# Kernel optimization log

Hardware: AMD Instinct MI355X
Metric: run time of the kernel (lower is better)

## Reference

```python
import jax, jax.numpy as jnp
import numpy as np

EPS = 0.5      # sinkhorn eps used by assign_batch_sinkhorn
NITERS = 15    # sinkhorn iterations used by assign_batch_sinkhorn


def pairwise_dists(features, centroids):
    # ||f - c|| via the expansion ||f||^2 + ||c||^2 - 2 f.c (avoids the
    # [B, nc, D] intermediate the naive broadcast would materialize).
    f2 = jnp.sum(features * features, axis=-1)          # [B]
    c2 = jnp.sum(centroids * centroids, axis=-1)        # [K]
    d2 = f2[:, None] + c2[None, :] - 2.0 * features @ centroids.T  # [B, K]
    return jnp.sqrt(jnp.maximum(d2, 0.0))


def sinkhorn(scores, eps=EPS, niters=NITERS):
    # Faithful to the torch sinkhorn(): Q = exp(scores/eps).T, normalize
    # columns (sum over K), then alternate row/column scalings.
    Q = jnp.exp(scores / eps).T                          # [K, B]
    Q = Q / jnp.sum(Q, axis=0, keepdims=True)
    K, B = Q.shape
    r = jnp.ones((K,), Q.dtype) / K
    c = jnp.ones((B,), Q.dtype) / B

    def body(_, Q):
        Q = Q * (r / jnp.sum(Q, axis=1))[:, None]
        Q = Q * (c / jnp.sum(Q, axis=0))[None, :]
        return Q

    Q = jax.lax.fori_loop(0, niters, body, Q)
    return (Q / jnp.sum(Q, axis=0, keepdims=True)).T     # [B, K]


def setup_inputs() -> dict:
    key = jax.random.key(0)
    kf, kc = jax.random.split(key)
    B, K, D = 16384, 2048, 1000
    # 0.1 scale keeps dists ~O(5) so exp(-dists/eps) stays in fp32 range
    # (unit-randn 1000-dim features give dists ~45 -> exp underflow).
    features = 0.1 * jax.random.normal(kf, (B, D), dtype=jnp.float32)
    centroids = 0.1 * jax.random.normal(kc, (K, D), dtype=jnp.float32)
    return {"features": features, "centroids": centroids}


def reference(features, centroids):
    B, K = features.shape[0], centroids.shape[0]
    dists = pairwise_dists(features, centroids)          # [B, K]

    # assign_batch_sinkhorn (soft assignments computed under no_grad)
    soft = jax.lax.stop_gradient(sinkhorn(-dists))       # [B, K]
    batch_assignments = jnp.argmin(soft, axis=1)         # [B] (as in source)
    soft_counts = jnp.sum(soft, axis=0)                  # [K]
    cluster_loss = jnp.mean(
        jnp.take_along_axis(dists, batch_assignments[:, None], axis=1))

    # the per-element python count loops, as fused scatter-adds
    cluster_counts = jnp.zeros((K,), jnp.int32).at[batch_assignments].add(1)
    raw_assign = jnp.argmin(dists, axis=1)
    raw_counts = jnp.zeros((K,), jnp.int32).at[raw_assign].add(1)

    return cluster_loss, batch_assignments, soft_counts, cluster_counts, raw_counts
```

## Files before the change

### kernel.cpp

```cpp
#include <hip/hip_runtime.h>

typedef __attribute__((ext_vector_type(8))) short bf16x8;
typedef __attribute__((ext_vector_type(8))) unsigned short ushort8_t;
typedef __attribute__((ext_vector_type(4))) float f32x4;

#define NB 16384
#define NK 2048
#define ND 1000
#define KP 1024
#define NCHK 1024

__device__ ushort g_E[(size_t)NB * NK];
__device__ ushort g_R[(size_t)NB * NK];
__device__ ushort g_Fh[(size_t)NB * KP], g_Fl[(size_t)NB * KP];
__device__ ushort g_Ch[(size_t)NK * KP], g_Cl[(size_t)NK * KP];
__device__ float  g_u[NK], g_c2[NK];
__device__ float  g_f2[NB], g_bd[NB];
__device__ float  g_part[(size_t)NCHK * NK];
__device__ int    g_cc[NK], g_rc[NK];

typedef const __attribute__((address_space(1))) void gvoid_t;
typedef __attribute__((address_space(3))) void lvoid_t;

union h16 { ushort u; _Float16 h; };

__device__ __forceinline__ ushort bf16_rne(float x){
    uint u = __float_as_uint(x);
    uint lsb = (u >> 16) & 1u;
    u += 0x7fffu + lsb;
    return (ushort)(u >> 16);
}
__device__ __forceinline__ float bf16_to_f(ushort h){
    return __uint_as_float(((uint)h) << 16);
}

__global__ __launch_bounds__(256) void cn_prep(const float* __restrict__ F,
                                               const float* __restrict__ Cn){
    const int isC = (blockIdx.x >= NB);
    const int row = isC ? (blockIdx.x - NB) : blockIdx.x;
    const float* __restrict__ X = isC ? Cn : F;
    ushort* __restrict__ H = isC ? g_Ch : g_Fh;
    ushort* __restrict__ L = isC ? g_Cl : g_Fl;
    float*  __restrict__ sq = isC ? g_c2 : g_f2;
    const int t = threadIdx.x;
    const int lane = t & 63, wid = t >> 6;
    if (isC && t == 0){ g_cc[row] = 0; g_rc[row] = 0; }
    float4 x = make_float4(0.f,0.f,0.f,0.f);
    if (t < 250) x = *(const float4*)(X + (size_t)row * ND + 4 * t);
    double s = (double)x.x*x.x + (double)x.y*x.y + (double)x.z*x.z + (double)x.w*x.w;
    ushort4 h4, l4;
#pragma unroll
    for (int c = 0; c < 4; ++c){
        float xc = (&x.x)[c];
        ushort h = bf16_rne(xc);
        (&h4.x)[c] = h;
        (&l4.x)[c] = bf16_rne(xc - bf16_to_f(h));
    }
    const int base = (t >> 3) << 5;
    const int grp  = (t >> 1) & 3;
    const int pos  = base + ((grp ^ ((row >> 1) & 3)) << 3) + ((4 * t) & 7);
    *(ushort4*)&H[(size_t)row * KP + pos] = h4;
    *(ushort4*)&L[(size_t)row * KP + pos] = l4;

    __shared__ double pr[4];
    for (int off = 32; off; off >>= 1) s += __shfl_xor(s, off);
    if (lane == 0) pr[wid] = s;
    __syncthreads();
    if (t == 0) sq[row] = (float)(pr[0] + pr[1] + pr[2] + pr[3]);
}

__global__ __launch_bounds__(256) void cn_gemm_dist(){
    __shared__ __attribute__((aligned(16))) ushort Ah[128 * 32];
    __shared__ __attribute__((aligned(16))) ushort Al[128 * 32];
    __shared__ __attribute__((aligned(16))) ushort Bh[128 * 32];
    __shared__ __attribute__((aligned(16))) ushort Bl[128 * 32];

    const int tid = threadIdx.x;
    const int lane = tid & 63, wid = tid >> 6;
    const int wr = wid >> 1, wc = wid & 1;
    const int brow0 = blockIdx.y * 128, bcol0 = blockIdx.x * 128;

    f32x4 acc[4][4];
#pragma unroll
    for (int m = 0; m < 4; ++m)
#pragma unroll
        for (int n = 0; n < 4; ++n) acc[m][n] = (f32x4){0.f,0.f,0.f,0.f};

    const int lrow = lane >> 2;
    const int lcol = (lane & 3) * 8;

    for (int step = 0; step < 32; ++step){
        const int k0 = step * 32;
#pragma unroll
        for (int i = 0; i < 2; ++i){
            const int ch = wid * 2 + i;
            const int ldso = ch * 512;
            const size_t ga = ((size_t)(brow0 + ch * 16 + lrow)) * KP + k0 + lcol;
            const size_t gb = ((size_t)(bcol0 + ch * 16 + lrow)) * KP + k0 + lcol;
            __builtin_amdgcn_global_load_lds((gvoid_t*)(g_Fh + ga), (lvoid_t*)(Ah + ldso), 16, 0, 0);
            __builtin_amdgcn_global_load_lds((gvoid_t*)(g_Fl + ga), (lvoid_t*)(Al + ldso), 16, 0, 0);
            __builtin_amdgcn_global_load_lds((gvoid_t*)(g_Ch + gb), (lvoid_t*)(Bh + ldso), 16, 0, 0);
            __builtin_amdgcn_global_load_lds((gvoid_t*)(g_Cl + gb), (lvoid_t*)(Bl + ldso), 16, 0, 0);
        }
        __syncthreads();

        const int arow = wr * 64 + (lane & 15);
        const int brow = wc * 64 + (lane & 15);
        const int kof  = (((lane >> 4) ^ ((lane >> 1) & 3)) * 8);
        bf16x8 afh[4], afl[4], bfh[4], bfl[4];
#pragma unroll
        for (int m = 0; m < 4; ++m){
            afh[m] = *(const bf16x8*)&Ah[(arow + m * 16) * 32 + kof];
            afl[m] = *(const bf16x8*)&Al[(arow + m * 16) * 32 + kof];
        }
#pragma unroll
        for (int n = 0; n < 4; ++n){
            bfh[n] = *(const bf16x8*)&Bh[(brow + n * 16) * 32 + kof];
            bfl[n] = *(const bf16x8*)&Bl[(brow + n * 16) * 32 + kof];
        }
#pragma unroll
        for (int m = 0; m < 4; ++m)
#pragma unroll
            for (int n = 0; n < 4; ++n){
                acc[m][n] = __builtin_amdgcn_mfma_f32_16x16x32_bf16(afh[m], bfh[n], acc[m][n], 0, 0, 0);
                acc[m][n] = __builtin_amdgcn_mfma_f32_16x16x32_bf16(afh[m], bfl[n], acc[m][n], 0, 0, 0);
                acc[m][n] = __builtin_amdgcn_mfma_f32_16x16x32_bf16(afl[m], bfh[n], acc[m][n], 0, 0, 0);
            }
        __syncthreads();
    }

#pragma unroll
    for (int m = 0; m < 4; ++m){
        int rowb = brow0 + wr * 64 + m * 16 + (lane >> 4) * 4;
#pragma unroll
        for (int n = 0; n < 4; ++n){
            int col = bcol0 + wc * 64 + n * 16 + (lane & 15);
            float c2v = g_c2[col];
#pragma unroll
            for (int j = 0; j < 4; ++j){
                float d2 = g_f2[rowb + j] + c2v - 2.0f * acc[m][n][j];
                float d  = sqrtf(fmaxf(d2, 0.0f));
                float e32 = __expf(-2.0f * d) * 8192.0f;
                size_t idx = (size_t)(rowb + j) * NK + col;
                h16 hv; hv.h = (_Float16)e32;
                float hf = (float)hv.h;
                h16 rv; rv.h = (_Float16)(e32 - hf);
                g_E[idx] = hv.u;
                g_R[idx] = rv.u;
            }
        }
    }
}

template<int MODE>
__global__ __launch_bounds__(256) void cn_sweep(float* __restrict__ outba){
    __shared__ float4 sred[3][8][64];
    const int lane = threadIdx.x & 63, wid = threadIdx.x >> 6;
    const int row0 = (blockIdx.x * 4 + wid) * 4;
    const float cst = (MODE == 0) ? 1.0f : (1.0f / (float)NB);

    float4 uu[8];
    if (MODE >= 1){
#pragma unroll
        for (int j = 0; j < 4; ++j)
#pragma unroll
            for (int h = 0; h < 2; ++h)
                uu[2 * j + h] = *(const float4*)&g_u[512 * j + 8 * lane + 4 * h];
    }

    float4 S[8];
#pragma unroll
    for (int j = 0; j < 8; ++j) S[j] = make_float4(0.f,0.f,0.f,0.f);

    for (int r = 0; r < 4; ++r){
        const int b = row0 + r;
        float tsum = 0.f;
        if (MODE <= 1){
            ushort8_t q8[4];
            const ushort* er = g_E + (size_t)b * NK + 8 * lane;
#pragma unroll
            for (int j = 0; j < 4; ++j){
                q8[j] = *(const ushort8_t*)(er + 512 * j);
#pragma unroll
                for (int c = 0; c < 8; ++c){
                    h16 cv; cv.u = q8[j][c];
                    float e = (float)cv.h;
                    tsum += (MODE == 1) ? e * (&uu[2 * j + (c >> 2)].x)[c & 3] : e;
                }
            }
#pragma unroll
            for (int off = 32; off; off >>= 1) tsum += __shfl_xor(tsum, off);
            const float v = cst / tsum;
#pragma unroll
            for (int j = 0; j < 4; ++j)
#pragma unroll
                for (int c = 0; c < 8; ++c){
                    h16 cv; cv.u = q8[j][c];
                    (&S[2 * j + (c >> 2)].x)[c & 3] += (float)cv.h * v;
                }
        } else {
            float ev[4][8];
            const ushort* er = g_E + (size_t)b * NK + 8 * lane;
            const ushort* rr = g_R + (size_t)b * NK + 8 * lane;
#pragma unroll
            for (int j = 0; j < 4; ++j){
                ushort8_t qe = *(const ushort8_t*)(er + 512 * j);
                ushort8_t qr = *(const ushort8_t*)(rr + 512 * j);
#pragma unroll
                for (int c = 0; c < 8; ++c){
                    h16 cv; cv.u = qe[c];
                    h16 rv; rv.u = qr[c];
                    float e = (float)cv.h + (float)rv.h;
                    ev[j][c] = e;
                    tsum += e * (&uu[2 * j + (c >> 2)].x)[c & 3];
                }
            }
#pragma unroll
            for (int off = 32; off; off >>= 1) tsum += __shfl_xor(tsum, off);
            const float v = cst / tsum;
#pragma unroll
            for (int j = 0; j < 4; ++j)
#pragma unroll
                for (int c = 0; c < 8; ++c)
                    (&S[2 * j + (c >> 2)].x)[c & 3] += ev[j][c] * v;

            if (MODE == 3){
                double bestW = 1.0e300; int bi = 0; float be = 1.f;
                float rbe = -1.f;      int ri = 0;
#pragma unroll
                for (int j = 0; j < 4; ++j){
#pragma unroll
                    for (int c = 0; c < 8; ++c){
                        int k = 512 * j + 8 * lane + c;
                        float e = ev[j][c];
                        double w = (double)e * (double)(&uu[2 * j + (c >> 2)].x)[c & 3];
                        if (w < bestW){ bestW = w; bi = k; be = e; }
                        if (e > rbe){ rbe = e; ri = k; }
                    }
                }
                for (int off = 32; off; off >>= 1){
                    double oW = __shfl_xor(bestW, off);
                    int    oi = __shfl_xor(bi, off);
                    float  oe = __shfl_xor(be, off);
                    if (oW < bestW || (oW == bestW && oi < bi)){ bestW = oW; bi = oi; be = oe; }
                    float ore = __shfl_xor(rbe, off);
                    int   ori = __shfl_xor(ri, off);
                    if (ore > rbe || (ore == rbe && ori < ri)){ rbe = ore; ri = ori; }
                }
                if (lane == 0){
                    outba[b] = (float)bi;
                    g_bd[b] = (float)(-0.5 * (log((double)be) - 9.010913347279288));
                    atomicAdd(&g_cc[bi], 1);
                    atomicAdd(&g_rc[ri], 1);
                }
            }
        }
    }

    if (wid > 0){
#pragma unroll
        for (int j = 0; j < 8; ++j) sred[wid - 1][j][lane] = S[j];
    }
    __syncthreads();
    if (wid == 0){
#pragma unroll
        for (int w = 0; w < 3; ++w)
#pragma unroll
            for (int j = 0; j < 8; ++j){
                float4 o = sred[w][j][lane];
                S[j].x += o.x; S[j].y += o.y; S[j].z += o.z; S[j].w += o.w;
            }
#pragma unroll
        for (int j = 0; j < 4; ++j)
#pragma unroll
            for (int h = 0; h < 2; ++h)
                *(float4*)&g_part[(size_t)blockIdx.x * NK + 512 * j + 8 * lane + 4 * h] = S[2 * j + h];
    }
}

__global__ __launch_bounds__(256) void cn_red0(){
    __shared__ double red[4][8];
    const int kk  = threadIdx.x & 7;
    const int sub = threadIdx.x >> 3;
    const int wv  = threadIdx.x >> 6;
    const int k = blockIdx.x * 8 + kk;
    double s = 0.0;
#pragma unroll 8
    for (int i = 0; i < 32; ++i)
        s += (double)g_part[(size_t)(i * 32 + sub) * NK + k];
    s += __shfl_xor(s, 8); s += __shfl_xor(s, 16); s += __shfl_xor(s, 32);
    if ((threadIdx.x & 63) < 8) red[wv][kk] = s;
    __syncthreads();
    if (threadIdx.x < 8){
        double tot = red[0][kk] + red[1][kk] + red[2][kk] + red[3][kk];
        g_u[blockIdx.x * 8 + kk] = (float)((1.0 / (double)NK) / tot);
    }
}

__global__ __launch_bounds__(256) void cn_fin(float* __restrict__ out){
    __shared__ double red[4][64];
    __shared__ double lred[4];
    const int lane = threadIdx.x & 63, q = threadIdx.x >> 6;
    const int k = blockIdx.x * 64 + lane;
    double s = 0.0;
    for (int ch = q * 256; ch < q * 256 + 256; ++ch)
        s += (double)g_part[(size_t)ch * NK + k];
    red[q][lane] = s;
    __syncthreads();
    if (q == 0){
        double tot = red[0][lane] + red[1][lane] + red[2][lane] + red[3][lane];
        out[1 + NB + k] = (float)((double)NB * (double)g_u[k] * tot);
    } else if (q == 1){
        out[1 + NB + NK + k] = (float)g_cc[k];
    } else if (q == 2){
        out[1 + NB + 2 * NK + k] = (float)g_rc[k];
    }
    if (blockIdx.x == 0){
        double sl = 0.0;
        for (int b = threadIdx.x; b < NB; b += 256) sl += (double)g_bd[b];
        for (int off = 32; off; off >>= 1) sl += __shfl_xor(sl, off);
        if (lane == 0) lred[q] = sl;
        __syncthreads();
        if (threadIdx.x == 0)
            out[0] = (float)((lred[0] + lred[1] + lred[2] + lred[3]) / (double)NB);
    }
}

extern "C" void kernel_launch(void* const* d_in, const int* in_sizes, int n_in,
                              void* d_out, int out_size, void* d_ws, size_t ws_size,
                              hipStream_t stream){
    const float* F  = (const float*)d_in[0];
    const float* Cn = (const float*)d_in[1];
    float* out = (float*)d_out;
    (void)d_ws; (void)ws_size;

    cn_prep<<<NB + NK, 256, 0, stream>>>(F, Cn);

    dim3 gg(NK / 128, NB / 128);
    cn_gemm_dist<<<gg, 256, 0, stream>>>();

    cn_sweep<0><<<NCHK, 256, 0, stream>>>(nullptr);
    cn_red0<<<NK / 8, 256, 0, stream>>>();
    for (int it = 1; it <= 11; ++it){
        cn_sweep<1><<<NCHK, 256, 0, stream>>>(nullptr);
        cn_red0<<<NK / 8, 256, 0, stream>>>();
    }
    for (int it = 12; it <= 14; ++it){
        cn_sweep<2><<<NCHK, 256, 0, stream>>>(nullptr);
        cn_red0<<<NK / 8, 256, 0, stream>>>();
    }
    cn_sweep<3><<<NCHK, 256, 0, stream>>>(out + 1);
    cn_fin<<<NK / 64, 256, 0, stream>>>(out);
}
```

Measured before the change: 722.7 us.

## Switch distance GEMM to 32x32x16 MFMA with 64-wide K tiles and swizzle

Replaces the 16x16x32 bf16 MFMA tiling with 32x32x16 MFMA instructions, using 2x2 f32x16 accumulators per wave. The K tile per step grows from 32 to 64, halving loop iterations and barriers, and the LDS swizzle used by the preprocessing kernel is rewritten for the 64-wide rows. The aim is fewer LDS fragment loads per MFMA and less synchronisation overhead. In exchange LDS use per block doubles, which may reduce occupancy, and the epilogue row mapping changes.

```diff
diff --git a/kernel.cpp b/kernel.cpp
--- a/kernel.cpp
+++ b/kernel.cpp
@@ -3,6 +3,7 @@
 typedef __attribute__((ext_vector_type(8))) short bf16x8;
 typedef __attribute__((ext_vector_type(8))) unsigned short ushort8_t;
 typedef __attribute__((ext_vector_type(4))) float f32x4;
+typedef __attribute__((ext_vector_type(16))) float f32x16;
 
 #define NB 16384
 #define NK 2048
@@ -56,9 +57,9 @@
         (&h4.x)[c] = h;
         (&l4.x)[c] = bf16_rne(xc - bf16_to_f(h));
     }
-    const int base = (t >> 3) << 5;
-    const int grp  = (t >> 1) & 3;
-    const int pos  = base + ((grp ^ ((row >> 1) & 3)) << 3) + ((4 * t) & 7);
+    const int base = (t >> 4) << 6;
+    const int grp  = (t >> 1) & 7;
+    const int pos  = base + ((grp ^ (row & 7)) << 3) + ((4 * t) & 7);
     *(ushort4*)&H[(size_t)row * KP + pos] = h4;
     *(ushort4*)&L[(size_t)row * KP + pos] = l4;
 
@@ -70,33 +71,40 @@
 }
 
 __global__ __launch_bounds__(256) void cn_gemm_dist(){
-    __shared__ __attribute__((aligned(16))) ushort Ah[128 * 32];
-    __shared__ __attribute__((aligned(16))) ushort Al[128 * 32];
-    __shared__ __attribute__((aligned(16))) ushort Bh[128 * 32];
-    __shared__ __attribute__((aligned(16))) ushort Bl[128 * 32];
+    __shared__ __attribute__((aligned(16))) ushort Ah[128 * 64];
+    __shared__ __attribute__((aligned(16))) ushort Al[128 * 64];
+    __shared__ __attribute__((aligned(16))) ushort Bh[128 * 64];
+    __shared__ __attribute__((aligned(16))) ushort Bl[128 * 64];
 
     const int tid = threadIdx.x;
     const int lane = tid & 63, wid = tid >> 6;
     const int wr = wid >> 1, wc = wid & 1;
     const int brow0 = blockIdx.y * 128, bcol0 = blockIdx.x * 128;
 
-    f32x4 acc[4][4];
-#pragma unroll
-    for (int m = 0; m < 4; ++m)
-#pragma unroll
-        for (int n = 0; n < 4; ++n) acc[m][n] = (f32x4){0.f,0.f,0.f,0.f};
-
-    const int lrow = lane >> 2;
-    const int lcol = (lane & 3) * 8;
-
-    for (int step = 0; step < 32; ++step){
-        const int k0 = step * 32;
-#pragma unroll
-        for (int i = 0; i < 2; ++i){
-            const int ch = wid * 2 + i;
+    f32x16 acc[2][2];
+#pragma unroll
+    for (int mt = 0; mt < 2; ++mt)
+#pragma unroll
+        for (int nt = 0; nt < 2; ++nt)
+#pragma unroll
+            for (int r = 0; r < 16; ++r) acc[mt][nt][r] = 0.f;
+
+    const int srow = lane >> 3;
+    const int sgr  = lane & 7;
+
+    const int arow = wr * 64 + (lane & 31);
+    const int brow = wc * 64 + (lane & 31);
+    const int kh   = lane >> 5;
+    const int rx   = lane & 7;
+
+    for (int kt = 0; kt < 16; ++kt){
+        const int k0 = kt * 64;
+#pragma unroll
+        for (int c4 = 0; c4 < 4; ++c4){
+            const int ch = wid * 4 + c4;
             const int ldso = ch * 512;
-            const size_t ga = ((size_t)(brow0 + ch * 16 + lrow)) * KP + k0 + lcol;
-            const size_t gb = ((size_t)(bcol0 + ch * 16 + lrow)) * KP + k0 + lcol;
+            const size_t ga = (size_t)(brow0 + ch * 8 + srow) * KP + k0 + sgr * 8;
+            const size_t gb = (size_t)(bcol0 + ch * 8 + srow) * KP + k0 + sgr * 8;
             __builtin_amdgcn_global_load_lds((gvoid_t*)(g_Fh + ga), (lvoid_t*)(Ah + ldso), 16, 0, 0);
             __builtin_amdgcn_global_load_lds((gvoid_t*)(g_Fl + ga), (lvoid_t*)(Al + ldso), 16, 0, 0);
             __builtin_amdgcn_global_load_lds((gvoid_t*)(g_Ch + gb), (lvoid_t*)(Bh + ldso), 16, 0, 0);
@@ -104,44 +112,47 @@
         }
         __syncthreads();
 
-        const int arow = wr * 64 + (lane & 15);
-        const int brow = wc * 64 + (lane & 15);
-        const int kof  = (((lane >> 4) ^ ((lane >> 1) & 3)) * 8);
-        bf16x8 afh[4], afl[4], bfh[4], bfl[4];
-#pragma unroll
-        for (int m = 0; m < 4; ++m){
-            afh[m] = *(const bf16x8*)&Ah[(arow + m * 16) * 32 + kof];
-            afl[m] = *(const bf16x8*)&Al[(arow + m * 16) * 32 + kof];
+#pragma unroll
+        for (int ks = 0; ks < 4; ++ks){
+            const int pg = (ks * 2 + kh) ^ rx;
+            bf16x8 a_h[2], a_l[2], b_h[2], b_l[2];
+#pragma unroll
+            for (int mt = 0; mt < 2; ++mt){
+                const int ro = (arow + mt * 32) * 64 + pg * 8;
+                a_h[mt] = *(const bf16x8*)&Ah[ro];
+                a_l[mt] = *(const bf16x8*)&Al[ro];
+            }
+#pragma unroll
+            for (int nt = 0; nt < 2; ++nt){
+                const int ro = (brow + nt * 32) * 64 + pg * 8;
+                b_h[nt] = *(const bf16x8*)&Bh[ro];
+                b_l[nt] = *(const bf16x8*)&Bl[ro];
+            }
+#pragma unroll
+            for (int mt = 0; mt < 2; ++mt)
+#pragma unroll
+                for (int nt = 0; nt < 2; ++nt){
+                    acc[mt][nt] = __builtin_amdgcn_mfma_f32_32x32x16_bf16(a_h[mt], b_h[nt], acc[mt][nt], 0, 0, 0);
+                    acc[mt][nt] = __builtin_amdgcn_mfma_f32_32x32x16_bf16(a_h[mt], b_l[nt], acc[mt][nt], 0, 0, 0);
+                    acc[mt][nt] = __builtin_amdgcn_mfma_f32_32x32x16_bf16(a_l[mt], b_h[nt], acc[mt][nt], 0, 0, 0);
+                }
         }
-#pragma unroll
-        for (int n = 0; n < 4; ++n){
-            bfh[n] = *(const bf16x8*)&Bh[(brow + n * 16) * 32 + kof];
-            bfl[n] = *(const bf16x8*)&Bl[(brow + n * 16) * 32 + kof];
-        }
-#pragma unroll
-        for (int m = 0; m < 4; ++m)
-#pragma unroll
-            for (int n = 0; n < 4; ++n){
-                acc[m][n] = __builtin_amdgcn_mfma_f32_16x16x32_bf16(afh[m], bfh[n], acc[m][n], 0, 0, 0);
-                acc[m][n] = __builtin_amdgcn_mfma_f32_16x16x32_bf16(afh[m], bfl[n], acc[m][n], 0, 0, 0);
-                acc[m][n] = __builtin_amdgcn_mfma_f32_16x16x32_bf16(afl[m], bfh[n], acc[m][n], 0, 0, 0);
-            }
         __syncthreads();
     }
 
 #pragma unroll
-    for (int m = 0; m < 4; ++m){
-        int rowb = brow0 + wr * 64 + m * 16 + (lane >> 4) * 4;
-#pragma unroll
-        for (int n = 0; n < 4; ++n){
-            int col = bcol0 + wc * 64 + n * 16 + (lane & 15);
-            float c2v = g_c2[col];
-#pragma unroll
-            for (int j = 0; j < 4; ++j){
-                float d2 = g_f2[rowb + j] + c2v - 2.0f * acc[m][n][j];
+    for (int mt = 0; mt < 2; ++mt){
+#pragma unroll
+        for (int nt = 0; nt < 2; ++nt){
+            const int col = bcol0 + wc * 64 + nt * 32 + (lane & 31);
+            const float c2v = g_c2[col];
+#pragma unroll
+            for (int reg = 0; reg < 16; ++reg){
+                const int row = brow0 + wr * 64 + mt * 32 + (reg & 3) + 8 * (reg >> 2) + 4 * kh;
+                float d2 = g_f2[row] + c2v - 2.0f * acc[mt][nt][reg];
                 float d  = sqrtf(fmaxf(d2, 0.0f));
                 float e32 = __expf(-2.0f * d) * 8192.0f;
-                size_t idx = (size_t)(rowb + j) * NK + col;
+                size_t idx = (size_t)row * NK + col;
                 h16 hv; hv.h = (_Float16)e32;
                 float hf = (float)hv.h;
                 h16 rv; rv.h = (_Float16)(e32 - hf);
```

After: 704.6 us. 1.03x faster.
